# Kernel optimization log

Measured on AMD Instinct MI355X. Metric: run time of the kernel, lower is better.

Reference implementation:

```python
import jax, jax.numpy as jnp
import numpy as np

LEAK = 0.01  # torch F.leaky_relu default
EPS = 1e-5   # torch LayerNorm default


def _ln(x, g, b):
    mu = jnp.mean(x, axis=-1, keepdims=True)
    var = jnp.var(x, axis=-1, keepdims=True)
    return (x - mu) * jax.lax.rsqrt(var + EPS) * g + b


def setup_inputs() -> dict:
    key = jax.random.key(0)
    ks = jax.random.split(key, 12)
    npeds, h, e = 8192, 256, 64
    s = 0.05
    return {
        "last_pos": jax.random.normal(ks[0], (npeds, 2), jnp.float32),
        "last_pos_rel": jax.random.normal(ks[1], (npeds, 2), jnp.float32),
        "h0": jax.random.normal(ks[2], (1, npeds, h), jnp.float32) * s,
        "c0": jax.random.normal(ks[3], (1, npeds, h), jnp.float32) * s,
        "W_ih": jax.random.normal(ks[4], (4 * h, e), jnp.float32) * s,
        "W_hh": jax.random.normal(ks[5], (4 * h, h), jnp.float32) * s,
        "b_ih": jax.random.normal(ks[6], (4 * h,), jnp.float32) * s,
        "b_hh": jax.random.normal(ks[7], (4 * h,), jnp.float32) * s,
        "emb_W": jax.random.normal(ks[8], (e, 2), jnp.float32) * s,
        "emb_b": jax.random.normal(ks[9], (e,), jnp.float32) * s,
        "ln1_g": jnp.ones((2,), jnp.float32),
        "ln1_b": jnp.zeros((2,), jnp.float32),
        "pos_W": jax.random.normal(ks[10], (2, h), jnp.float32) * s,
        "pos_b": jax.random.normal(ks[11], (2,), jnp.float32) * s,
        "ln2_g": jnp.ones((h,), jnp.float32),
        "ln2_b": jnp.zeros((h,), jnp.float32),
    }


def reference(last_pos, last_pos_rel, h0, c0, W_ih, W_hh, b_ih, b_hh,
              emb_W, emb_b, ln1_g, ln1_b, pos_W, pos_b, ln2_g, ln2_b):
    seq_len = 30
    h_dim = W_hh.shape[1]
    bias = b_ih + b_hh

    def embed(p):  # leaky_relu(spatial_embedding(ln1(p)))
        return jax.nn.leaky_relu(_ln(p, ln1_g, ln1_b) @ emb_W.T + emb_b, LEAK)

    def step(carry, _):
        dec_in, h, c, lp = carry  # dec_in [N,e], h/c [N,H], lp [N,2]
        gates = dec_in @ W_ih.T + h @ W_hh.T + bias  # [N,4H]
        i, f, g, o = jnp.split(gates, 4, axis=-1)    # torch gate order i,f,g,o
        c = jax.nn.sigmoid(f) * c + jax.nn.sigmoid(i) * jnp.tanh(g)
        h = jax.nn.sigmoid(o) * jnp.tanh(c)
        rel = jax.nn.sigmoid(_ln(h, ln2_g, ln2_b) @ pos_W.T + pos_b)  # [N,2]
        lp = rel + lp
        return (embed(rel), h, c, lp), rel

    carry0 = (embed(last_pos_rel), h0[0], c0[0], last_pos)
    _, rels = jax.lax.scan(step, carry0, None, length=seq_len)
    return rels  # [seq_len, npeds, 2]
```

## Files before the change

kernel.cpp:

```cpp
#include <hip/hip_runtime.h>


typedef float  f32x4  __attribute__((ext_vector_type(4)));
typedef short  short8 __attribute__((ext_vector_type(8)));
typedef __bf16 bf16x8 __attribute__((ext_vector_type(8)));
typedef int    i32x4  __attribute__((ext_vector_type(4)));

#define WS_W     0
#define WS_HBUF  (640 * 1024)
#define WS_SBUF  (WS_HBUF + 8388608)
#define WS_BIAS  (WS_SBUF + 524288)
#define WS_SCAL  (WS_BIAS + 4096)
#define WS_CTR   (WS_SCAL + 64)

__device__ __forceinline__ unsigned short f2bf(float f) {
  unsigned int u = __float_as_uint(f);
  u += 0x7FFFu + ((u >> 16) & 1u);
  return (unsigned short)(u >> 16);
}
__device__ __forceinline__ float sigm(float x) {
  return __builtin_amdgcn_rcpf(1.0f + __expf(-x));
}
__device__ __forceinline__ float tanh_(float x) {
  float ax = fabsf(x);
  float t = __expf(-2.0f * ax);
  float r = (1.0f - t) * __builtin_amdgcn_rcpf(1.0f + t);
  return x >= 0.0f ? r : -r;
}
__device__ __forceinline__ f32x4 mfma16(short8 a, short8 b, f32x4 c) {
  return __builtin_amdgcn_mfma_f32_16x16x32_bf16(
      __builtin_bit_cast(bf16x8, a), __builtin_bit_cast(bf16x8, b), c, 0, 0, 0);
}
__device__ __forceinline__ void sc_store16(void* p, i32x4 v) {
  asm volatile("global_store_dwordx4 %0, %1, off sc0 sc1" ::"v"(p), "v"(v)
               : "memory");
}
__device__ __forceinline__ void drain_vm() {
  asm volatile("s_waitcnt vmcnt(0)" ::: "memory");
}
__device__ __forceinline__ void batch_load3(const i32x4* p0, const i32x4* p1,
                                            const i32x4* p2, i32x4& r0,
                                            i32x4& r1, i32x4& r2) {
  asm volatile(
      "global_load_dwordx4 %0, %3, off sc0 sc1\n\t"
      "global_load_dwordx4 %1, %4, off sc0 sc1\n\t"
      "global_load_dwordx4 %2, %5, off sc0 sc1\n\t"
      "s_waitcnt vmcnt(0)"
      : "=&v"(r0), "=&v"(r1), "=&v"(r2)
      : "v"(p0), "v"(p1), "v"(p2)
      : "memory");
}

extern "C" __global__ void shuffle_weights(const float* __restrict__ Wih,
                                           const float* __restrict__ Whh,
                                           unsigned short* __restrict__ ws_w) {
  int t = blockIdx.x * 256 + threadIdx.x;
  if (t >= 40960) return;
  int l = t & 63;
  int g = (t >> 6) & 3;
  int w8 = (t >> 8) & 7;
  int y = t >> 11;
  int kc = y % 10;
  int ug = y / 10;
  int row = g * 256 + ug * 128 + w8 * 16 + (l & 15);
  unsigned short* dst = ws_w + (size_t)t * 8;
  if (kc < 2) {
    const float* src = Wih + row * 64 + kc * 32 + (l >> 4) * 8;
#pragma unroll
    for (int j = 0; j < 8; j++) dst[j] = f2bf(src[j]);
  } else {
    const float* src = Whh + row * 256 + (kc - 2) * 32 + (l >> 4) * 8;
#pragma unroll
    for (int j = 0; j < 8; j++) dst[j] = f2bf(src[j]);
  }
}

extern "C" __global__ void prologue2(const float* __restrict__ b_ih,
                                     const float* __restrict__ b_hh,
                                     const float* __restrict__ ln2g,
                                     const float* __restrict__ ln2b,
                                     const float* __restrict__ posW,
                                     float* __restrict__ biasv,
                                     float* __restrict__ scal,
                                     int* __restrict__ ctr) {
  int t = threadIdx.x;
#pragma unroll
  for (int k2 = 0; k2 < 4; k2++) {
    int n = t * 4 + k2;
    biasv[n] = b_ih[n] + b_hh[n];
  }
  if (t < 128) ctr[t * 64] = 0;
  __shared__ float red[256][4];
  float g = ln2g[t], b = ln2b[t], p0 = posW[t], p1 = posW[256 + t];
  red[t][0] = b * p0;
  red[t][1] = b * p1;
  red[t][2] = g * p0;
  red[t][3] = g * p1;
  __syncthreads();
  for (int s = 128; s > 0; s >>= 1) {
    if (t < s) {
#pragma unroll
      for (int v = 0; v < 4; v++) red[t][v] += red[t + s][v];
    }
    __syncthreads();
  }
  if (t == 0) {
#pragma unroll
    for (int v = 0; v < 4; v++) scal[v] = red[0][v];
  }
}

extern "C" __global__ __launch_bounds__(512, 2) void decoder_main(
    const float* __restrict__ lpr, const float* __restrict__ h0,
    const float* __restrict__ c0, const float* __restrict__ embW,
    const float* __restrict__ embB, const float* __restrict__ ln1g,
    const float* __restrict__ ln1b, const float* __restrict__ posW,
    const float* __restrict__ posB, const float* __restrict__ ln2g,
    const unsigned short* __restrict__ ws_w,
    unsigned short* __restrict__ hbuf,
    float* __restrict__ sbuf,
    const float* __restrict__ biasv, const float* __restrict__ scal,
    int* __restrict__ ctr, float* __restrict__ out) {
  __shared__ unsigned short w_lds[3 * 8 * 4 * 512];
  __shared__ unsigned short h_stage[4 * 8 * 512];
  __shared__ unsigned short xh[4 * 2 * 512];
  __shared__ float partials[64 * 8 * 4];
  __shared__ float statl[64 * 4];
  __shared__ float n01[64][2];

  const int bid = blockIdx.x;
  const int pg = bid >> 1, ug = bid & 1;
  const int tid = threadIdx.x;
  const int w = tid >> 6, l = tid & 63;
  const int q = l >> 4, li = l & 15;
  const int P0 = pg * 64;
  const int loff = l * 8;
  const int u = ug * 128 + w * 16 + li;

  {
    const unsigned short* src = ws_w + (size_t)ug * 163840;
#pragma unroll
    for (int it = 0; it < 12; it++) {
      int f = tid + it * 512;
      *(short8*)(w_lds + f * 8) = *(const short8*)(src + f * 8);
    }
  }
  short8 wr[7][4];
#pragma unroll
  for (int kk = 0; kk < 7; kk++)
#pragma unroll
    for (int g = 0; g < 4; g++)
      wr[kk][g] = *(const short8*)(ws_w + (size_t)ug * 163840 +
                                   (((kk + 3) * 8 + w) * 4 + g) * 512 + loff);

  const float K0 = scal[0], K1 = scal[1], SP0 = scal[2], SP1 = scal[3];
  const float pb0 = posB[0], pb1 = posB[1];
  const float g10 = ln1g[0], g11 = ln1g[1], b10 = ln1b[0], b11 = ln1b[1];

  float bias_r[4];
#pragma unroll
  for (int g = 0; g < 4; g++) bias_r[g] = biasv[g * 256 + u];
  float Pp0, Pp1;
  {
    float gg = ln2g[u];
    Pp0 = gg * posW[u];
    Pp1 = gg * posW[256 + u];
  }

  f32x4 c_r[4];
#pragma unroll
  for (int mt = 0; mt < 4; mt++)
#pragma unroll
    for (int r = 0; r < 4; r++)
      c_r[mt][r] = c0[(size_t)(P0 + mt * 16 + q * 4 + r) * 256 + u];

#pragma unroll
  for (int it = 0; it < 4; it++) {
    int f = tid + it * 512;
    int ll = f & 63, kc = (f >> 6) & 7, Tl = f >> 9;
    const float* src =
        h0 + (size_t)(P0 + Tl * 16 + (ll & 15)) * 256 + kc * 32 + (ll >> 4) * 8;
    float tf[8];
    *(float4*)&tf[0] = *(const float4*)(src);
    *(float4*)&tf[4] = *(const float4*)(src + 4);
    short8 sv;
#pragma unroll
    for (int j = 0; j < 8; j++) sv[j] = (short)f2bf(tf[j]);
    *(short8*)(h_stage + f * 8) = sv;
  }

  if (tid < 64) {
    float r0 = lpr[(P0 + tid) * 2], r1 = lpr[(P0 + tid) * 2 + 1];
    float d = 0.5f * (r0 - r1);
    float rs = rsqrtf(d * d + 1e-5f);
    n01[tid][0] = d * rs * g10 + b10;
    n01[tid][1] = -d * rs * g11 + b11;
  }
  __syncthreads();

  {
    const int pc = tid >> 3, s8 = tid & 7;
    float n0 = n01[pc][0], n1 = n01[pc][1];
    int Tl = pc >> 4, row = pc & 15;
#pragma unroll
    for (int jj = 0; jj < 8; jj++) {
      int k = s8 * 8 + jj;
      float e = n0 * embW[k * 2] + n1 * embW[k * 2 + 1] + embB[k];
      e = e > 0.f ? e : 0.01f * e;
      xh[(Tl * 2 + (k >> 5)) * 512 + (row + 16 * ((k & 31) >> 3)) * 8 + (k & 7)] =
          f2bf(e);
    }
  }
  __syncthreads();

  i32x4* hb4 = (i32x4*)hbuf;
  i32x4* sb4 = (i32x4*)sbuf;
  i32x4* hs4 = (i32x4*)h_stage;
  const size_t own_base = ((size_t)pg * 2 + ug) * 1024;
  const size_t par_base = ((size_t)pg * 2 + (ug ^ 1)) * 1024;
  const size_t sown_base = ((size_t)pg * 2 + ug) * 64;
  const size_t spar_base = ((size_t)pg * 2 + (ug ^ 1)) * 64;

  for (int st = 0; st < 30; st++) {
    const size_t pbase = (size_t)(st & 1) * 262144;
    const size_t sbase = (size_t)(st & 1) * 16384;

    f32x4 acc[4][4];
#pragma unroll
    for (int g = 0; g < 4; g++)
#pragma unroll
      for (int mt = 0; mt < 4; mt++)
        acc[g][mt] = (f32x4){bias_r[g], bias_r[g], bias_r[g], bias_r[g]};

#pragma unroll
    for (int kc2 = 0; kc2 < 2; kc2++) {
      short8 ax[4];
#pragma unroll
      for (int mt = 0; mt < 4; mt++)
        ax[mt] = *(const short8*)(xh + (mt * 2 + kc2) * 512 + loff);
#pragma unroll
      for (int g = 0; g < 4; g++) {
        short8 b =
            *(const short8*)(w_lds + ((kc2 * 8 + w) * 4 + g) * 512 + loff);
#pragma unroll
        for (int mt = 0; mt < 4; mt++)
          acc[g][mt] = mfma16(ax[mt], b, acc[g][mt]);
      }
    }
#pragma unroll
    for (int kc = 0; kc < 8; kc++) {
      short8 a[4];
#pragma unroll
      for (int mt = 0; mt < 4; mt++)
        a[mt] = *(const short8*)(h_stage + (mt * 8 + kc) * 512 + loff);
      if (kc == 0) {
#pragma unroll
        for (int g = 0; g < 4; g++) {
          short8 b =
              *(const short8*)(w_lds + ((2 * 8 + w) * 4 + g) * 512 + loff);
#pragma unroll
          for (int mt = 0; mt < 4; mt++)
            acc[g][mt] = mfma16(a[mt], b, acc[g][mt]);
        }
      } else {
#pragma unroll
        for (int g = 0; g < 4; g++)
#pragma unroll
          for (int mt = 0; mt < 4; mt++)
            acc[g][mt] = mfma16(a[mt], wr[kc - 1][g], acc[g][mt]);
      }
    }
    __syncthreads();

#pragma unroll
    for (int mt = 0; mt < 4; mt++) {
      float sh[4], sh2[4], sA[4], sB[4];
#pragma unroll
      for (int r = 0; r < 4; r++) {
        float iv = sigm(acc[0][mt][r]);
        float fv = sigm(acc[1][mt][r]);
        float gv = tanh_(acc[2][mt][r]);
        float ov = sigm(acc[3][mt][r]);
        float cc = fv * c_r[mt][r] + iv * gv;
        c_r[mt][r] = cc;
        float hv = ov * tanh_(cc);
        h_stage[(mt * 8 + ug * 4 + (w >> 1)) * 512 +
                ((q * 4 + r) + 16 * ((w & 1) * 2 + (li >> 3))) * 8 + (li & 7)] =
            f2bf(hv);
        sh[r] = hv;
        sh2[r] = hv * hv;
        sA[r] = hv * Pp0;
        sB[r] = hv * Pp1;
      }
#pragma unroll
      for (int mask = 1; mask <= 8; mask <<= 1) {
#pragma unroll
        for (int r = 0; r < 4; r++) {
          sh[r] += __shfl_xor(sh[r], mask, 64);
          sh2[r] += __shfl_xor(sh2[r], mask, 64);
          sA[r] += __shfl_xor(sA[r], mask, 64);
          sB[r] += __shfl_xor(sB[r], mask, 64);
        }
      }
      if (li == 0) {
#pragma unroll
        for (int r = 0; r < 4; r++)
          *(f32x4*)(partials + ((mt * 16 + q * 4 + r) * 8 + w) * 4) =
              (f32x4){sh[r], sh2[r], sA[r], sB[r]};
      }
    }
    __syncthreads();

    f32x4 sown = (f32x4){0.f, 0.f, 0.f, 0.f};
    if (st < 29) {
#pragma unroll
      for (int it = 0; it < 2; it++) {
        int f = tid + it * 512;
        int c = f >> 6, rr = f & 63;
        int mt = c >> 2, kcl = c & 3;
        i32x4 v = hs4[(mt * 8 + ug * 4 + kcl) * 64 + rr];
        sc_store16(hb4 + pbase + own_base + f, v);
      }
    }
    if (tid < 64) {
      f32x4 sv = *(const f32x4*)(partials + tid * 32);
#pragma unroll
      for (int ww = 1; ww < 8; ww++) {
        f32x4 t2 = *(const f32x4*)(partials + (tid * 8 + ww) * 4);
        sv.x += t2.x; sv.y += t2.y; sv.z += t2.z; sv.w += t2.w;
      }
      sown = sv;
      sc_store16(sb4 + sbase + sown_base + tid, __builtin_bit_cast(i32x4, sv));
    }
    drain_vm();
    __syncthreads();

    if (tid == 0) {
      __hip_atomic_fetch_add(ctr + pg * 64, 1, __ATOMIC_RELAXED,
                             __HIP_MEMORY_SCOPE_AGENT);
      int target = 2 * (st + 1);
      while (__hip_atomic_load(ctr + pg * 64, __ATOMIC_RELAXED,
                               __HIP_MEMORY_SCOPE_AGENT) < target)
        __builtin_amdgcn_s_sleep(1);
    }
    __syncthreads();

    {
      const i32x4* p0 = hb4 + pbase + par_base + tid;
      const i32x4* p1 = p0 + 512;
      const i32x4* p2 =
          (tid < 64) ? (sb4 + sbase + spar_base + tid) : p0;
      i32x4 r0, r1, r2;
      batch_load3(p0, p1, p2, r0, r1, r2);
      if (st < 29) {
        int c0i = tid >> 6, rr = tid & 63;
        hs4[((c0i >> 2) * 8 + (ug ^ 1) * 4 + (c0i & 3)) * 64 + rr] = r0;
        int f1 = tid + 512;
        int c1 = f1 >> 6, rr1 = f1 & 63;
        hs4[((c1 >> 2) * 8 + (ug ^ 1) * 4 + (c1 & 3)) * 64 + rr1] = r1;
      }
      if (tid < 64) *(i32x4*)(statl + tid * 4) = __builtin_bit_cast(i32x4, r2);
    }
    __syncthreads();

    if (tid < 64) {
      f32x4 sp = *(const f32x4*)(statl + tid * 4);
      float S = sown.x + sp.x;
      float S2 = sown.y + sp.y;
      float D0 = sown.z + sp.z;
      float D1 = sown.w + sp.w;
      float mu = S * (1.0f / 256.0f);
      float var = S2 * (1.0f / 256.0f) - mu * mu;
      float rsig = rsqrtf(var + 1e-5f);
      float rel0 = sigm(rsig * (D0 - mu * SP0) + K0 + pb0);
      float rel1 = sigm(rsig * (D1 - mu * SP1) + K1 + pb1);
      if (ug == 0)
        *(float2*)(out + (size_t)st * 16384 + (P0 + tid) * 2) =
            make_float2(rel0, rel1);
      float d = 0.5f * (rel0 - rel1);
      float rs = rsqrtf(d * d + 1e-5f);
      n01[tid][0] = d * rs * g10 + b10;
      n01[tid][1] = -d * rs * g11 + b11;
    }
    __syncthreads();

    if (st < 29) {
      const int pc = tid >> 3, s8 = tid & 7;
      float n0 = n01[pc][0], n1 = n01[pc][1];
      int Tl = pc >> 4, row = pc & 15;
#pragma unroll
      for (int jj = 0; jj < 8; jj++) {
        int k = s8 * 8 + jj;
        float e = n0 * embW[k * 2] + n1 * embW[k * 2 + 1] + embB[k];
        e = e > 0.f ? e : 0.01f * e;
        xh[(Tl * 2 + (k >> 5)) * 512 + (row + 16 * ((k & 31) >> 3)) * 8 +
           (k & 7)] = f2bf(e);
      }
    }
    __syncthreads();
  }
}

extern "C" void kernel_launch(void* const* d_in, const int* in_sizes, int n_in,
                              void* d_out, int out_size, void* d_ws,
                              size_t ws_size, hipStream_t stream) {
  (void)in_sizes; (void)n_in; (void)out_size; (void)ws_size;
  const float* lpr  = (const float*)d_in[1];
  const float* h0   = (const float*)d_in[2];
  const float* c0   = (const float*)d_in[3];
  const float* Wih  = (const float*)d_in[4];
  const float* Whh  = (const float*)d_in[5];
  const float* b_ih = (const float*)d_in[6];
  const float* b_hh = (const float*)d_in[7];
  const float* embW = (const float*)d_in[8];
  const float* embB = (const float*)d_in[9];
  const float* ln1g = (const float*)d_in[10];
  const float* ln1b = (const float*)d_in[11];
  const float* posW = (const float*)d_in[12];
  const float* posB = (const float*)d_in[13];
  const float* ln2g = (const float*)d_in[14];
  const float* ln2b = (const float*)d_in[15];

  char* ws = (char*)d_ws;
  unsigned short* ws_w = (unsigned short*)(ws + WS_W);
  unsigned short* hbuf = (unsigned short*)(ws + WS_HBUF);
  float* sbufp  = (float*)(ws + WS_SBUF);
  float* biasv  = (float*)(ws + WS_BIAS);
  float* scal   = (float*)(ws + WS_SCAL);
  int*   ctr    = (int*)(ws + WS_CTR);

  shuffle_weights<<<dim3(160), dim3(256), 0, stream>>>(Wih, Whh, ws_w);
  prologue2<<<dim3(1), dim3(256), 0, stream>>>(b_ih, b_hh, ln2g, ln2b, posW,
                                               biasv, scal, ctr);
  decoder_main<<<dim3(256), dim3(512), 0, stream>>>(
      lpr, h0, c0, embW, embB, ln1g, ln1b, posW, posB, ln2g, ws_w, hbuf,
      sbufp, biasv, scal, ctr, (float*)d_out);
}
```

Before: 546.9 us.

## Give each block all hidden units for 32 peds, dropping cross-block exchange

```diff
diff --git a/kernel.cpp b/kernel.cpp
--- a/kernel.cpp
+++ b/kernel.cpp
@@ -4,14 +4,10 @@
 typedef float  f32x4  __attribute__((ext_vector_type(4)));
 typedef short  short8 __attribute__((ext_vector_type(8)));
 typedef __bf16 bf16x8 __attribute__((ext_vector_type(8)));
-typedef int    i32x4  __attribute__((ext_vector_type(4)));
 
 #define WS_W     0
-#define WS_HBUF  (640 * 1024)
-#define WS_SBUF  (WS_HBUF + 8388608)
-#define WS_BIAS  (WS_SBUF + 524288)
+#define WS_BIAS  (640 * 1024)
 #define WS_SCAL  (WS_BIAS + 4096)
-#define WS_CTR   (WS_SCAL + 64)
 
 __device__ __forceinline__ unsigned short f2bf(float f) {
   unsigned int u = __float_as_uint(f);
@@ -30,25 +26,6 @@
 __device__ __forceinline__ f32x4 mfma16(short8 a, short8 b, f32x4 c) {
   return __builtin_amdgcn_mfma_f32_16x16x32_bf16(
       __builtin_bit_cast(bf16x8, a), __builtin_bit_cast(bf16x8, b), c, 0, 0, 0);
-}
-__device__ __forceinline__ void sc_store16(void* p, i32x4 v) {
-  asm volatile("global_store_dwordx4 %0, %1, off sc0 sc1" ::"v"(p), "v"(v)
-               : "memory");
-}
-__device__ __forceinline__ void drain_vm() {
-  asm volatile("s_waitcnt vmcnt(0)" ::: "memory");
-}
-__device__ __forceinline__ void batch_load3(const i32x4* p0, const i32x4* p1,
-                                            const i32x4* p2, i32x4& r0,
-                                            i32x4& r1, i32x4& r2) {
-  asm volatile(
-      "global_load_dwordx4 %0, %3, off sc0 sc1\n\t"
-      "global_load_dwordx4 %1, %4, off sc0 sc1\n\t"
-      "global_load_dwordx4 %2, %5, off sc0 sc1\n\t"
-      "s_waitcnt vmcnt(0)"
-      : "=&v"(r0), "=&v"(r1), "=&v"(r2)
-      : "v"(p0), "v"(p1), "v"(p2)
-      : "memory");
 }
 
 extern "C" __global__ void shuffle_weights(const float* __restrict__ Wih,
@@ -57,22 +34,15 @@
   int t = blockIdx.x * 256 + threadIdx.x;
   if (t >= 40960) return;
   int l = t & 63;
-  int g = (t >> 6) & 3;
-  int w8 = (t >> 8) & 7;
-  int y = t >> 11;
-  int kc = y % 10;
-  int ug = y / 10;
-  int row = g * 256 + ug * 128 + w8 * 16 + (l & 15);
+  int nt = (t >> 6) & 63;
+  int kc = t >> 12;
+  int row = nt * 16 + (l & 15);
+  int cb = (l >> 4) * 8;
   unsigned short* dst = ws_w + (size_t)t * 8;
-  if (kc < 2) {
-    const float* src = Wih + row * 64 + kc * 32 + (l >> 4) * 8;
-#pragma unroll
-    for (int j = 0; j < 8; j++) dst[j] = f2bf(src[j]);
-  } else {
-    const float* src = Whh + row * 256 + (kc - 2) * 32 + (l >> 4) * 8;
-#pragma unroll
-    for (int j = 0; j < 8; j++) dst[j] = f2bf(src[j]);
-  }
+  const float* src = (kc < 2) ? (Wih + row * 64 + kc * 32 + cb)
+                              : (Whh + row * 256 + (kc - 2) * 32 + cb);
+#pragma unroll
+  for (int j = 0; j < 8; j++) dst[j] = f2bf(src[j]);
 }
 
 extern "C" __global__ void prologue2(const float* __restrict__ b_ih,
@@ -81,15 +51,13 @@
                                      const float* __restrict__ ln2b,
                                      const float* __restrict__ posW,
                                      float* __restrict__ biasv,
-                                     float* __restrict__ scal,
-                                     int* __restrict__ ctr) {
+                                     float* __restrict__ scal) {
   int t = threadIdx.x;
 #pragma unroll
   for (int k2 = 0; k2 < 4; k2++) {
     int n = t * 4 + k2;
     biasv[n] = b_ih[n] + b_hh[n];
   }
-  if (t < 128) ctr[t * 64] = 0;
   __shared__ float red[256][4];
   float g = ln2g[t], b = ln2b[t], p0 = posW[t], p1 = posW[256 + t];
   red[t][0] = b * p0;
@@ -117,69 +85,57 @@
     const float* __restrict__ ln1b, const float* __restrict__ posW,
     const float* __restrict__ posB, const float* __restrict__ ln2g,
     const unsigned short* __restrict__ ws_w,
-    unsigned short* __restrict__ hbuf,
-    float* __restrict__ sbuf,
     const float* __restrict__ biasv, const float* __restrict__ scal,
-    int* __restrict__ ctr, float* __restrict__ out) {
-  __shared__ unsigned short w_lds[3 * 8 * 4 * 512];
-  __shared__ unsigned short h_stage[4 * 8 * 512];
-  __shared__ unsigned short xh[4 * 2 * 512];
-  __shared__ float partials[64 * 8 * 4];
-  __shared__ float statl[64 * 4];
-  __shared__ float n01[64][2];
+    float* __restrict__ out) {
+  __shared__ unsigned short h_stage[16 * 512];
+  __shared__ unsigned short xh[4 * 512];
+  __shared__ float partials[32 * 8 * 4];
+  __shared__ float n01[32][2];
 
   const int bid = blockIdx.x;
-  const int pg = bid >> 1, ug = bid & 1;
   const int tid = threadIdx.x;
   const int w = tid >> 6, l = tid & 63;
   const int q = l >> 4, li = l & 15;
-  const int P0 = pg * 64;
+  const int P0 = bid * 32;
   const int loff = l * 8;
-  const int u = ug * 128 + w * 16 + li;
-
-  {
-    const unsigned short* src = ws_w + (size_t)ug * 163840;
-#pragma unroll
-    for (int it = 0; it < 12; it++) {
-      int f = tid + it * 512;
-      *(short8*)(w_lds + f * 8) = *(const short8*)(src + f * 8);
-    }
-  }
-  short8 wr[7][4];
-#pragma unroll
-  for (int kk = 0; kk < 7; kk++)
-#pragma unroll
-    for (int g = 0; g < 4; g++)
-      wr[kk][g] = *(const short8*)(ws_w + (size_t)ug * 163840 +
-                                   (((kk + 3) * 8 + w) * 4 + g) * 512 + loff);
+  const int u0 = w * 32 + li;
+
+  const unsigned short* wsw = ws_w + w * 1024 + loff;
 
   const float K0 = scal[0], K1 = scal[1], SP0 = scal[2], SP1 = scal[3];
   const float pb0 = posB[0], pb1 = posB[1];
   const float g10 = ln1g[0], g11 = ln1g[1], b10 = ln1b[0], b11 = ln1b[1];
 
-  float bias_r[4];
-#pragma unroll
-  for (int g = 0; g < 4; g++) bias_r[g] = biasv[g * 256 + u];
-  float Pp0, Pp1;
-  {
-    float gg = ln2g[u];
-    Pp0 = gg * posW[u];
-    Pp1 = gg * posW[256 + u];
-  }
-
-  f32x4 c_r[4];
-#pragma unroll
-  for (int mt = 0; mt < 4; mt++)
-#pragma unroll
-    for (int r = 0; r < 4; r++)
-      c_r[mt][r] = c0[(size_t)(P0 + mt * 16 + q * 4 + r) * 256 + u];
-
-#pragma unroll
-  for (int it = 0; it < 4; it++) {
+  float bias_r[4][2];
+#pragma unroll
+  for (int g = 0; g < 4; g++)
+#pragma unroll
+    for (int j = 0; j < 2; j++) bias_r[g][j] = biasv[g * 256 + u0 + j * 16];
+  float Pp0[2], Pp1[2];
+#pragma unroll
+  for (int j = 0; j < 2; j++) {
+    float gg = ln2g[u0 + j * 16];
+    Pp0[j] = gg * posW[u0 + j * 16];
+    Pp1[j] = gg * posW[256 + u0 + j * 16];
+  }
+
+  f32x4 c_r[2][2];
+#pragma unroll
+  for (int mt = 0; mt < 2; mt++)
+#pragma unroll
+    for (int j = 0; j < 2; j++)
+#pragma unroll
+      for (int r = 0; r < 4; r++)
+        c_r[mt][j][r] =
+            c0[(size_t)(P0 + mt * 16 + q * 4 + r) * 256 + u0 + j * 16];
+
+#pragma unroll
+  for (int it = 0; it < 2; it++) {
     int f = tid + it * 512;
-    int ll = f & 63, kc = (f >> 6) & 7, Tl = f >> 9;
-    const float* src =
-        h0 + (size_t)(P0 + Tl * 16 + (ll & 15)) * 256 + kc * 32 + (ll >> 4) * 8;
+    int ll = f & 63, fr = f >> 6;
+    int mt = fr >> 3, kc = fr & 7;
+    const float* src = h0 + (size_t)(P0 + mt * 16 + (ll & 15)) * 256 +
+                       kc * 32 + (ll >> 4) * 8;
     float tf[8];
     *(float4*)&tf[0] = *(const float4*)(src);
     *(float4*)&tf[4] = *(const float4*)(src + 4);
@@ -189,7 +145,7 @@
     *(short8*)(h_stage + f * 8) = sv;
   }
 
-  if (tid < 64) {
+  if (tid < 32) {
     float r0 = lpr[(P0 + tid) * 2], r1 = lpr[(P0 + tid) * 2 + 1];
     float d = 0.5f * (r0 - r1);
     float rs = rsqrtf(d * d + 1e-5f);
@@ -199,98 +155,91 @@
   __syncthreads();
 
   {
-    const int pc = tid >> 3, s8 = tid & 7;
+    const int pc = tid >> 4, s16 = tid & 15;
     float n0 = n01[pc][0], n1 = n01[pc][1];
-    int Tl = pc >> 4, row = pc & 15;
-#pragma unroll
-    for (int jj = 0; jj < 8; jj++) {
-      int k = s8 * 8 + jj;
+    int mt = pc >> 4, row = pc & 15;
+#pragma unroll
+    for (int jj = 0; jj < 4; jj++) {
+      int k = s16 * 4 + jj;
       float e = n0 * embW[k * 2] + n1 * embW[k * 2 + 1] + embB[k];
       e = e > 0.f ? e : 0.01f * e;
-      xh[(Tl * 2 + (k >> 5)) * 512 + (row + 16 * ((k & 31) >> 3)) * 8 + (k & 7)] =
-          f2bf(e);
+      xh[(mt * 2 + (k >> 5)) * 512 + (row + 16 * ((k & 31) >> 3)) * 8 +
+         (k & 7)] = f2bf(e);
     }
   }
   __syncthreads();
 
-  i32x4* hb4 = (i32x4*)hbuf;
-  i32x4* sb4 = (i32x4*)sbuf;
-  i32x4* hs4 = (i32x4*)h_stage;
-  const size_t own_base = ((size_t)pg * 2 + ug) * 1024;
-  const size_t par_base = ((size_t)pg * 2 + (ug ^ 1)) * 1024;
-  const size_t sown_base = ((size_t)pg * 2 + ug) * 64;
-  const size_t spar_base = ((size_t)pg * 2 + (ug ^ 1)) * 64;
+  short8 bb[2][4][2];
+#pragma unroll
+  for (int g = 0; g < 4; g++)
+#pragma unroll
+    for (int j = 0; j < 2; j++)
+      bb[0][g][j] = *(const short8*)(wsw + g * 8192 + j * 512);
 
   for (int st = 0; st < 30; st++) {
-    const size_t pbase = (size_t)(st & 1) * 262144;
-    const size_t sbase = (size_t)(st & 1) * 16384;
-
-    f32x4 acc[4][4];
-#pragma unroll
-    for (int g = 0; g < 4; g++)
-#pragma unroll
-      for (int mt = 0; mt < 4; mt++)
-        acc[g][mt] = (f32x4){bias_r[g], bias_r[g], bias_r[g], bias_r[g]};
-
-#pragma unroll
-    for (int kc2 = 0; kc2 < 2; kc2++) {
-      short8 ax[4];
-#pragma unroll
-      for (int mt = 0; mt < 4; mt++)
-        ax[mt] = *(const short8*)(xh + (mt * 2 + kc2) * 512 + loff);
-#pragma unroll
-      for (int g = 0; g < 4; g++) {
-        short8 b =
-            *(const short8*)(w_lds + ((kc2 * 8 + w) * 4 + g) * 512 + loff);
-#pragma unroll
-        for (int mt = 0; mt < 4; mt++)
-          acc[g][mt] = mfma16(ax[mt], b, acc[g][mt]);
-      }
-    }
-#pragma unroll
-    for (int kc = 0; kc < 8; kc++) {
-      short8 a[4];
-#pragma unroll
-      for (int mt = 0; mt < 4; mt++)
-        a[mt] = *(const short8*)(h_stage + (mt * 8 + kc) * 512 + loff);
-      if (kc == 0) {
-#pragma unroll
-        for (int g = 0; g < 4; g++) {
-          short8 b =
-              *(const short8*)(w_lds + ((2 * 8 + w) * 4 + g) * 512 + loff);
-#pragma unroll
-          for (int mt = 0; mt < 4; mt++)
-            acc[g][mt] = mfma16(a[mt], b, acc[g][mt]);
+    f32x4 acc[2][4][2];
+#pragma unroll
+    for (int mt = 0; mt < 2; mt++)
+#pragma unroll
+      for (int g = 0; g < 4; g++)
+#pragma unroll
+        for (int j = 0; j < 2; j++)
+          acc[mt][g][j] = (f32x4){bias_r[g][j], bias_r[g][j], bias_r[g][j],
+                                  bias_r[g][j]};
+
+#pragma unroll
+    for (int kc = 0; kc < 10; kc++) {
+      const int nkc = (kc == 9) ? 0 : kc + 1;
+      const unsigned short* wp = wsw + nkc * 32768;
+#pragma unroll
+      for (int g = 0; g < 4; g++)
+#pragma unroll
+        for (int j = 0; j < 2; j++)
+          bb[(kc + 1) & 1][g][j] = *(const short8*)(wp + g * 8192 + j * 512);
+      short8 a0, a1;
+      if (kc < 2) {
+        a0 = *(const short8*)(xh + kc * 512 + loff);
+        a1 = *(const short8*)(xh + (2 + kc) * 512 + loff);
+      } else {
+        a0 = *(const short8*)(h_stage + (kc - 2) * 512 + loff);
+        a1 = *(const short8*)(h_stage + (8 + kc - 2) * 512 + loff);
+      }
+#pragma unroll
+      for (int g = 0; g < 4; g++)
+#pragma unroll
+        for (int j = 0; j < 2; j++) {
+          acc[0][g][j] = mfma16(a0, bb[kc & 1][g][j], acc[0][g][j]);
+          acc[1][g][j] = mfma16(a1, bb[kc & 1][g][j], acc[1][g][j]);
         }
-      } else {
-#pragma unroll
-        for (int g = 0; g < 4; g++)
-#pragma unroll
-          for (int mt = 0; mt < 4; mt++)
-            acc[g][mt] = mfma16(a[mt], wr[kc - 1][g], acc[g][mt]);
-      }
-    }
-    __syncthreads();
-
-#pragma unroll
-    for (int mt = 0; mt < 4; mt++) {
+    }
+    __syncthreads();
+
+#pragma unroll
+    for (int mt = 0; mt < 2; mt++) {
       float sh[4], sh2[4], sA[4], sB[4];
 #pragma unroll
       for (int r = 0; r < 4; r++) {
-        float iv = sigm(acc[0][mt][r]);
-        float fv = sigm(acc[1][mt][r]);
-        float gv = tanh_(acc[2][mt][r]);
-        float ov = sigm(acc[3][mt][r]);
-        float cc = fv * c_r[mt][r] + iv * gv;
-        c_r[mt][r] = cc;
-        float hv = ov * tanh_(cc);
-        h_stage[(mt * 8 + ug * 4 + (w >> 1)) * 512 +
-                ((q * 4 + r) + 16 * ((w & 1) * 2 + (li >> 3))) * 8 + (li & 7)] =
-            f2bf(hv);
-        sh[r] = hv;
-        sh2[r] = hv * hv;
-        sA[r] = hv * Pp0;
-        sB[r] = hv * Pp1;
+        sh[r] = 0.f; sh2[r] = 0.f; sA[r] = 0.f; sB[r] = 0.f;
+      }
+#pragma unroll
+      for (int j = 0; j < 2; j++) {
+#pragma unroll
+        for (int r = 0; r < 4; r++) {
+          float iv = sigm(acc[mt][0][j][r]);
+          float fv = sigm(acc[mt][1][j][r]);
+          float gv = tanh_(acc[mt][2][j][r]);
+          float ov = sigm(acc[mt][3][j][r]);
+          float cc = fv * c_r[mt][j][r] + iv * gv;
+          c_r[mt][j][r] = cc;
+          float hv = ov * tanh_(cc);
+          h_stage[(mt * 8 + w) * 512 +
+                  ((q * 4 + r) + 16 * (j * 2 + (li >> 3))) * 8 + (li & 7)] =
+              f2bf(hv);
+          sh[r] += hv;
+          sh2[r] += hv * hv;
+          sA[r] += hv * Pp0[j];
+          sB[r] += hv * Pp1[j];
+        }
       }
 #pragma unroll
       for (int mask = 1; mask <= 8; mask <<= 1) {
@@ -311,72 +260,20 @@
     }
     __syncthreads();
 
-    f32x4 sown = (f32x4){0.f, 0.f, 0.f, 0.f};
-    if (st < 29) {
-#pragma unroll
-      for (int it = 0; it < 2; it++) {
-        int f = tid + it * 512;
-        int c = f >> 6, rr = f & 63;
-        int mt = c >> 2, kcl = c & 3;
-        i32x4 v = hs4[(mt * 8 + ug * 4 + kcl) * 64 + rr];
-        sc_store16(hb4 + pbase + own_base + f, v);
-      }
-    }
-    if (tid < 64) {
+    if (tid < 32) {
       f32x4 sv = *(const f32x4*)(partials + tid * 32);
 #pragma unroll
       for (int ww = 1; ww < 8; ww++) {
         f32x4 t2 = *(const f32x4*)(partials + (tid * 8 + ww) * 4);
         sv.x += t2.x; sv.y += t2.y; sv.z += t2.z; sv.w += t2.w;
       }
-      sown = sv;
-      sc_store16(sb4 + sbase + sown_base + tid, __builtin_bit_cast(i32x4, sv));
-    }
-    drain_vm();
-    __syncthreads();
-
-    if (tid == 0) {
-      __hip_atomic_fetch_add(ctr + pg * 64, 1, __ATOMIC_RELAXED,
-                             __HIP_MEMORY_SCOPE_AGENT);
-      int target = 2 * (st + 1);
-      while (__hip_atomic_load(ctr + pg * 64, __ATOMIC_RELAXED,
-                               __HIP_MEMORY_SCOPE_AGENT) < target)
-        __builtin_amdgcn_s_sleep(1);
-    }
-    __syncthreads();
-
-    {
-      const i32x4* p0 = hb4 + pbase + par_base + tid;
-      const i32x4* p1 = p0 + 512;
-      const i32x4* p2 =
-          (tid < 64) ? (sb4 + sbase + spar_base + tid) : p0;
-      i32x4 r0, r1, r2;
-      batch_load3(p0, p1, p2, r0, r1, r2);
-      if (st < 29) {
-        int c0i = tid >> 6, rr = tid & 63;
-        hs4[((c0i >> 2) * 8 + (ug ^ 1) * 4 + (c0i & 3)) * 64 + rr] = r0;
-        int f1 = tid + 512;
-        int c1 = f1 >> 6, rr1 = f1 & 63;
-        hs4[((c1 >> 2) * 8 + (ug ^ 1) * 4 + (c1 & 3)) * 64 + rr1] = r1;
-      }
-      if (tid < 64) *(i32x4*)(statl + tid * 4) = __builtin_bit_cast(i32x4, r2);
-    }
-    __syncthreads();
-
-    if (tid < 64) {
-      f32x4 sp = *(const f32x4*)(statl + tid * 4);
-      float S = sown.x + sp.x;
-      float S2 = sown.y + sp.y;
-      float D0 = sown.z + sp.z;
-      float D1 = sown.w + sp.w;
-      float mu = S * (1.0f / 256.0f);
-      float var = S2 * (1.0f / 256.0f) - mu * mu;
+      float mu = sv.x * (1.0f / 256.0f);
+      float var = sv.y * (1.0f / 256.0f) - mu * mu;
       float rsig = rsqrtf(var + 1e-5f);
-      float rel0 = sigm(rsig * (D0 - mu * SP0) + K0 + pb0);
-      float rel1 = sigm(rsig * (D1 - mu * SP1) + K1 + pb1);
-      if (ug == 0)
-        *(float2*)(out + (size_t)st * 16384 + (P0 + tid) * 2) =
-            make_float2(rel0, rel1);
+      float rel0 = sigm(rsig * (sv.z - mu * SP0) + K0 + pb0);
+      float rel1 = sigm(rsig * (sv.w - mu * SP1) + K1 + pb1);
+      *(float2*)(out + (size_t)st * 16384 + (P0 + tid) * 2) =
+          make_float2(rel0, rel1);
       float d = 0.5f * (rel0 - rel1);
       float rs = rsqrtf(d * d + 1e-5f);
       n01[tid][0] = d * rs * g10 + b10;
@@ -384,16 +281,16 @@
     }
     __syncthreads();
 
-    if (st < 29) {
-      const int pc = tid >> 3, s8 = tid & 7;
+    {
+      const int pc = tid >> 4, s16 = tid & 15;
       float n0 = n01[pc][0], n1 = n01[pc][1];
-      int Tl = pc >> 4, row = pc & 15;
-#pragma unroll
-      for (int jj = 0; jj < 8; jj++) {
-        int k = s8 * 8 + jj;
+      int mt = pc >> 4, row = pc & 15;
+#pragma unroll
+      for (int jj = 0; jj < 4; jj++) {
+        int k = s16 * 4 + jj;
         float e = n0 * embW[k * 2] + n1 * embW[k * 2 + 1] + embB[k];
         e = e > 0.f ? e : 0.01f * e;
-        xh[(Tl * 2 + (k >> 5)) * 512 + (row + 16 * ((k & 31) >> 3)) * 8 +
+        xh[(mt * 2 + (k >> 5)) * 512 + (row + 16 * ((k & 31) >> 3)) * 8 +
            (k & 7)] = f2bf(e);
       }
     }
@@ -423,16 +320,13 @@
 
   char* ws = (char*)d_ws;
   unsigned short* ws_w = (unsigned short*)(ws + WS_W);
-  unsigned short* hbuf = (unsigned short*)(ws + WS_HBUF);
-  float* sbufp  = (float*)(ws + WS_SBUF);
   float* biasv  = (float*)(ws + WS_BIAS);
   float* scal   = (float*)(ws + WS_SCAL);
-  int*   ctr    = (int*)(ws + WS_CTR);
 
   shuffle_weights<<<dim3(160), dim3(256), 0, stream>>>(Wih, Whh, ws_w);
   prologue2<<<dim3(1), dim3(256), 0, stream>>>(b_ih, b_hh, ln2g, ln2b, posW,
-                                               biasv, scal, ctr);
+                                               biasv, scal);
   decoder_main<<<dim3(256), dim3(512), 0, stream>>>(
-      lpr, h0, c0, embW, embB, ln1g, ln1b, posW, posB, ln2g, ws_w, hbuf,
-      sbufp, biasv, scal, ctr, (float*)d_out);
-}
+      lpr, h0, c0, embW, embB, ln1g, ln1b, posW, posB, ln2g, ws_w, biasv,
+      scal, (float*)d_out);
+}
```

Result: slower. 907.8 us (+66.0%).

## Overlap own-half recurrent MFMAs with partner exchange wait via per-block tags

Applied to the files above, without the earlier changes.

```diff
diff --git a/kernel.cpp b/kernel.cpp
--- a/kernel.cpp
+++ b/kernel.cpp
@@ -34,6 +34,12 @@
 __device__ __forceinline__ void sc_store16(void* p, i32x4 v) {
   asm volatile("global_store_dwordx4 %0, %1, off sc0 sc1" ::"v"(p), "v"(v)
                : "memory");
+}
+__device__ __forceinline__ void sc_load16(const i32x4* p, i32x4& r) {
+  asm volatile(
+      "global_load_dwordx4 %0, %1, off sc0 sc1\n\t"
+      "s_waitcnt vmcnt(0)"
+      : "=v"(r) : "v"(p) : "memory");
 }
 __device__ __forceinline__ void drain_vm() {
   asm volatile("s_waitcnt vmcnt(0)" ::: "memory");
@@ -89,7 +95,7 @@
     int n = t * 4 + k2;
     biasv[n] = b_ih[n] + b_hh[n];
   }
-  if (t < 128) ctr[t * 64] = 0;
+  ctr[t * 32] = 0;
   __shared__ float red[256][4];
   float g = ln2g[t], b = ln2b[t], p0 = posW[t], p1 = posW[256 + t];
   red[t][0] = b * p0;
@@ -109,6 +115,21 @@
     for (int v = 0; v < 4; v++) scal[v] = red[0][v];
   }
 }
+
+#define MF_STAGE(A0, A1, A2, A3, BGET)                                     \
+  {                                                                        \
+    short8 a0_ = (A0), a1_ = (A1), a2_ = (A2), a3_ = (A3);                 \
+    _Pragma("unroll") for (int g_ = 0; g_ < 4; g_++) {                     \
+      short8 b_ = (BGET);                                                  \
+      acc[g_][0] = mfma16(a0_, b_, acc[g_][0]);                            \
+      acc[g_][1] = mfma16(a1_, b_, acc[g_][1]);                            \
+      acc[g_][2] = mfma16(a2_, b_, acc[g_][2]);                            \
+      acc[g_][3] = mfma16(a3_, b_, acc[g_][3]);                            \
+    }                                                                      \
+  }
+#define HSA(kh, mt) (*(const short8*)(h_stage + ((mt)*8 + (kh)) * 512 + loff))
+#define XA(k2, mt)  (*(const short8*)(xh + ((mt)*2 + (k2)) * 512 + loff))
+#define WL(kc, g)   (*(const short8*)(w_lds + (((kc)*8 + w) * 4 + (g)) * 512 + loff))
 
 extern "C" __global__ __launch_bounds__(512, 2) void decoder_main(
     const float* __restrict__ lpr, const float* __restrict__ h0,
@@ -125,11 +146,11 @@
   __shared__ unsigned short h_stage[4 * 8 * 512];
   __shared__ unsigned short xh[4 * 2 * 512];
   __shared__ float partials[64 * 8 * 4];
-  __shared__ float statl[64 * 4];
   __shared__ float n01[64][2];
 
   const int bid = blockIdx.x;
-  const int pg = bid >> 1, ug = bid & 1;
+  const int ug = (bid >> 3) & 1;
+  const int pg = (bid & 7) | ((bid >> 4) << 3);
   const int tid = threadIdx.x;
   const int w = tid >> 6, l = tid & 63;
   const int q = l >> 4, li = l & 15;
@@ -180,12 +201,13 @@
     int ll = f & 63, kc = (f >> 6) & 7, Tl = f >> 9;
     const float* src =
         h0 + (size_t)(P0 + Tl * 16 + (ll & 15)) * 256 + kc * 32 + (ll >> 4) * 8;
-    float tf[8];
-    *(float4*)&tf[0] = *(const float4*)(src);
-    *(float4*)&tf[4] = *(const float4*)(src + 4);
+    float4 ta = *(const float4*)(src);
+    float4 tb = *(const float4*)(src + 4);
     short8 sv;
-#pragma unroll
-    for (int j = 0; j < 8; j++) sv[j] = (short)f2bf(tf[j]);
+    sv[0] = (short)f2bf(ta.x); sv[1] = (short)f2bf(ta.y);
+    sv[2] = (short)f2bf(ta.z); sv[3] = (short)f2bf(ta.w);
+    sv[4] = (short)f2bf(tb.x); sv[5] = (short)f2bf(tb.y);
+    sv[6] = (short)f2bf(tb.z); sv[7] = (short)f2bf(tb.w);
     *(short8*)(h_stage + f * 8) = sv;
   }
 
@@ -220,11 +242,11 @@
   const size_t par_base = ((size_t)pg * 2 + (ug ^ 1)) * 1024;
   const size_t sown_base = ((size_t)pg * 2 + ug) * 64;
   const size_t spar_base = ((size_t)pg * 2 + (ug ^ 1)) * 64;
+  int* tag_own = ctr + (pg * 2 + ug) * 32;
+  int* tag_par = ctr + (pg * 2 + (ug ^ 1)) * 32;
+  f32x4 sown = (f32x4){0.f, 0.f, 0.f, 0.f};
 
   for (int st = 0; st < 30; st++) {
-    const size_t pbase = (size_t)(st & 1) * 262144;
-    const size_t sbase = (size_t)(st & 1) * 16384;
-
     f32x4 acc[4][4];
 #pragma unroll
     for (int g = 0; g < 4; g++)
@@ -232,45 +254,86 @@
       for (int mt = 0; mt < 4; mt++)
         acc[g][mt] = (f32x4){bias_r[g], bias_r[g], bias_r[g], bias_r[g]};
 
-#pragma unroll
-    for (int kc2 = 0; kc2 < 2; kc2++) {
-      short8 ax[4];
-#pragma unroll
-      for (int mt = 0; mt < 4; mt++)
-        ax[mt] = *(const short8*)(xh + (mt * 2 + kc2) * 512 + loff);
-#pragma unroll
-      for (int g = 0; g < 4; g++) {
-        short8 b =
-            *(const short8*)(w_lds + ((kc2 * 8 + w) * 4 + g) * 512 + loff);
-#pragma unroll
-        for (int mt = 0; mt < 4; mt++)
-          acc[g][mt] = mfma16(ax[mt], b, acc[g][mt]);
-      }
-    }
-#pragma unroll
-    for (int kc = 0; kc < 8; kc++) {
-      short8 a[4];
-#pragma unroll
-      for (int mt = 0; mt < 4; mt++)
-        a[mt] = *(const short8*)(h_stage + (mt * 8 + kc) * 512 + loff);
-      if (kc == 0) {
-#pragma unroll
-        for (int g = 0; g < 4; g++) {
-          short8 b =
-              *(const short8*)(w_lds + ((2 * 8 + w) * 4 + g) * 512 + loff);
-#pragma unroll
-          for (int mt = 0; mt < 4; mt++)
-            acc[g][mt] = mfma16(a[mt], b, acc[g][mt]);
+    if (ug == 0) {
+      MF_STAGE(HSA(0, 0), HSA(0, 1), HSA(0, 2), HSA(0, 3), WL(2, g_));
+      MF_STAGE(HSA(1, 0), HSA(1, 1), HSA(1, 2), HSA(1, 3), wr[0][g_]);
+      MF_STAGE(HSA(2, 0), HSA(2, 1), HSA(2, 2), HSA(2, 3), wr[1][g_]);
+      MF_STAGE(HSA(3, 0), HSA(3, 1), HSA(3, 2), HSA(3, 3), wr[2][g_]);
+    } else {
+      MF_STAGE(HSA(4, 0), HSA(4, 1), HSA(4, 2), HSA(4, 3), wr[3][g_]);
+      MF_STAGE(HSA(5, 0), HSA(5, 1), HSA(5, 2), HSA(5, 3), wr[4][g_]);
+      MF_STAGE(HSA(6, 0), HSA(6, 1), HSA(6, 2), HSA(6, 3), wr[5][g_]);
+      MF_STAGE(HSA(7, 0), HSA(7, 1), HSA(7, 2), HSA(7, 3), wr[6][g_]);
+    }
+
+    if (st > 0) {
+      while (__hip_atomic_load(tag_par, __ATOMIC_RELAXED,
+                               __HIP_MEMORY_SCOPE_AGENT) < st)
+        __builtin_amdgcn_s_sleep(1);
+      const size_t pbase = (size_t)((st - 1) & 1) * 262144;
+      const size_t sbase = (size_t)((st - 1) & 1) * 16384;
+      const i32x4* p0 = hb4 + pbase + par_base + tid;
+      const i32x4* p1 = p0 + 512;
+      const i32x4* p2 = (tid < 64) ? (sb4 + sbase + spar_base + tid) : p0;
+      i32x4 r0, r1, r2;
+      batch_load3(p0, p1, p2, r0, r1, r2);
+      {
+        int c0i = tid >> 6, rr = tid & 63;
+        hs4[((c0i >> 2) * 8 + (ug ^ 1) * 4 + (c0i & 3)) * 64 + rr] = r0;
+        int f1 = tid + 512;
+        int c1 = f1 >> 6, rr1 = f1 & 63;
+        hs4[((c1 >> 2) * 8 + (ug ^ 1) * 4 + (c1 & 3)) * 64 + rr1] = r1;
+      }
+      if (tid < 64) {
+        f32x4 sp = __builtin_bit_cast(f32x4, r2);
+        float S = sown.x + sp.x;
+        float S2 = sown.y + sp.y;
+        float D0 = sown.z + sp.z;
+        float D1 = sown.w + sp.w;
+        float mu = S * (1.0f / 256.0f);
+        float var = S2 * (1.0f / 256.0f) - mu * mu;
+        float rsig = rsqrtf(var + 1e-5f);
+        float rel0 = sigm(rsig * (D0 - mu * SP0) + K0 + pb0);
+        float rel1 = sigm(rsig * (D1 - mu * SP1) + K1 + pb1);
+        if (ug == 0)
+          *(float2*)(out + (size_t)(st - 1) * 16384 + (P0 + tid) * 2) =
+              make_float2(rel0, rel1);
+        float d = 0.5f * (rel0 - rel1);
+        float rs = rsqrtf(d * d + 1e-5f);
+        n01[tid][0] = d * rs * g10 + b10;
+        n01[tid][1] = -d * rs * g11 + b11;
+      }
+      __syncthreads();
+      {
+        const int pc = tid >> 3, s8 = tid & 7;
+        float n0 = n01[pc][0], n1 = n01[pc][1];
+        int Tl = pc >> 4, row = pc & 15;
+#pragma unroll
+        for (int jj = 0; jj < 8; jj++) {
+          int k = s8 * 8 + jj;
+          float e = n0 * embW[k * 2] + n1 * embW[k * 2 + 1] + embB[k];
+          e = e > 0.f ? e : 0.01f * e;
+          xh[(Tl * 2 + (k >> 5)) * 512 + (row + 16 * ((k & 31) >> 3)) * 8 +
+             (k & 7)] = f2bf(e);
         }
-      } else {
-#pragma unroll
-        for (int g = 0; g < 4; g++)
-#pragma unroll
-          for (int mt = 0; mt < 4; mt++)
-            acc[g][mt] = mfma16(a[mt], wr[kc - 1][g], acc[g][mt]);
-      }
-    }
-    __syncthreads();
+      }
+      __syncthreads();
+    }
+
+    MF_STAGE(XA(0, 0), XA(0, 1), XA(0, 2), XA(0, 3), WL(0, g_));
+    MF_STAGE(XA(1, 0), XA(1, 1), XA(1, 2), XA(1, 3), WL(1, g_));
+    if (ug == 0) {
+      MF_STAGE(HSA(4, 0), HSA(4, 1), HSA(4, 2), HSA(4, 3), wr[3][g_]);
+      MF_STAGE(HSA(5, 0), HSA(5, 1), HSA(5, 2), HSA(5, 3), wr[4][g_]);
+      MF_STAGE(HSA(6, 0), HSA(6, 1), HSA(6, 2), HSA(6, 3), wr[5][g_]);
+      MF_STAGE(HSA(7, 0), HSA(7, 1), HSA(7, 2), HSA(7, 3), wr[6][g_]);
+    } else {
+      MF_STAGE(HSA(0, 0), HSA(0, 1), HSA(0, 2), HSA(0, 3), WL(2, g_));
+      MF_STAGE(HSA(1, 0), HSA(1, 1), HSA(1, 2), HSA(1, 3), wr[0][g_]);
+      MF_STAGE(HSA(2, 0), HSA(2, 1), HSA(2, 2), HSA(2, 3), wr[1][g_]);
+      MF_STAGE(HSA(3, 0), HSA(3, 1), HSA(3, 2), HSA(3, 3), wr[2][g_]);
+    }
+    if (st == 0) __syncthreads();
 
 #pragma unroll
     for (int mt = 0; mt < 4; mt++) {
@@ -311,93 +374,57 @@
     }
     __syncthreads();
 
-    f32x4 sown = (f32x4){0.f, 0.f, 0.f, 0.f};
-    if (st < 29) {
-#pragma unroll
-      for (int it = 0; it < 2; it++) {
-        int f = tid + it * 512;
-        int c = f >> 6, rr = f & 63;
-        int mt = c >> 2, kcl = c & 3;
-        i32x4 v = hs4[(mt * 8 + ug * 4 + kcl) * 64 + rr];
-        sc_store16(hb4 + pbase + own_base + f, v);
-      }
-    }
-    if (tid < 64) {
-      f32x4 sv = *(const f32x4*)(partials + tid * 32);
-#pragma unroll
-      for (int ww = 1; ww < 8; ww++) {
-        f32x4 t2 = *(const f32x4*)(partials + (tid * 8 + ww) * 4);
-        sv.x += t2.x; sv.y += t2.y; sv.z += t2.z; sv.w += t2.w;
-      }
-      sown = sv;
-      sc_store16(sb4 + sbase + sown_base + tid, __builtin_bit_cast(i32x4, sv));
-    }
-    drain_vm();
-    __syncthreads();
-
-    if (tid == 0) {
-      __hip_atomic_fetch_add(ctr + pg * 64, 1, __ATOMIC_RELAXED,
-                             __HIP_MEMORY_SCOPE_AGENT);
-      int target = 2 * (st + 1);
-      while (__hip_atomic_load(ctr + pg * 64, __ATOMIC_RELAXED,
-                               __HIP_MEMORY_SCOPE_AGENT) < target)
-        __builtin_amdgcn_s_sleep(1);
-    }
-    __syncthreads();
-
     {
-      const i32x4* p0 = hb4 + pbase + par_base + tid;
-      const i32x4* p1 = p0 + 512;
-      const i32x4* p2 =
-          (tid < 64) ? (sb4 + sbase + spar_base + tid) : p0;
-      i32x4 r0, r1, r2;
-      batch_load3(p0, p1, p2, r0, r1, r2);
+      const size_t pbase_w = (size_t)(st & 1) * 262144;
+      const size_t sbase_w = (size_t)(st & 1) * 16384;
       if (st < 29) {
-        int c0i = tid >> 6, rr = tid & 63;
-        hs4[((c0i >> 2) * 8 + (ug ^ 1) * 4 + (c0i & 3)) * 64 + rr] = r0;
-        int f1 = tid + 512;
-        int c1 = f1 >> 6, rr1 = f1 & 63;
-        hs4[((c1 >> 2) * 8 + (ug ^ 1) * 4 + (c1 & 3)) * 64 + rr1] = r1;
-      }
-      if (tid < 64) *(i32x4*)(statl + tid * 4) = __builtin_bit_cast(i32x4, r2);
-    }
-    __syncthreads();
-
-    if (tid < 64) {
-      f32x4 sp = *(const f32x4*)(statl + tid * 4);
-      float S = sown.x + sp.x;
-      float S2 = sown.y + sp.y;
-      float D0 = sown.z + sp.z;
-      float D1 = sown.w + sp.w;
-      float mu = S * (1.0f / 256.0f);
-      float var = S2 * (1.0f / 256.0f) - mu * mu;
-      float rsig = rsqrtf(var + 1e-5f);
-      float rel0 = sigm(rsig * (D0 - mu * SP0) + K0 + pb0);
-      float rel1 = sigm(rsig * (D1 - mu * SP1) + K1 + pb1);
-      if (ug == 0)
-        *(float2*)(out + (size_t)st * 16384 + (P0 + tid) * 2) =
-            make_float2(rel0, rel1);
-      float d = 0.5f * (rel0 - rel1);
-      float rs = rsqrtf(d * d + 1e-5f);
-      n01[tid][0] = d * rs * g10 + b10;
-      n01[tid][1] = -d * rs * g11 + b11;
-    }
-    __syncthreads();
-
-    if (st < 29) {
-      const int pc = tid >> 3, s8 = tid & 7;
-      float n0 = n01[pc][0], n1 = n01[pc][1];
-      int Tl = pc >> 4, row = pc & 15;
-#pragma unroll
-      for (int jj = 0; jj < 8; jj++) {
-        int k = s8 * 8 + jj;
-        float e = n0 * embW[k * 2] + n1 * embW[k * 2 + 1] + embB[k];
-        e = e > 0.f ? e : 0.01f * e;
-        xh[(Tl * 2 + (k >> 5)) * 512 + (row + 16 * ((k & 31) >> 3)) * 8 +
-           (k & 7)] = f2bf(e);
-      }
-    }
-    __syncthreads();
+#pragma unroll
+        for (int it = 0; it < 2; it++) {
+          int f = tid + it * 512;
+          int c = f >> 6, rr = f & 63;
+          int mt = c >> 2, kcl = c & 3;
+          i32x4 v = hs4[(mt * 8 + ug * 4 + kcl) * 64 + rr];
+          sc_store16(hb4 + pbase_w + own_base + f, v);
+        }
+      }
+      if (tid < 64) {
+        f32x4 sv = *(const f32x4*)(partials + tid * 32);
+#pragma unroll
+        for (int ww = 1; ww < 8; ww++) {
+          f32x4 t2 = *(const f32x4*)(partials + (tid * 8 + ww) * 4);
+          sv.x += t2.x; sv.y += t2.y; sv.z += t2.z; sv.w += t2.w;
+        }
+        sown = sv;
+        sc_store16(sb4 + sbase_w + sown_base + tid,
+                   __builtin_bit_cast(i32x4, sv));
+      }
+      drain_vm();
+      __syncthreads();
+      if (tid == 0)
+        __hip_atomic_store(tag_own, st + 1, __ATOMIC_RELAXED,
+                           __HIP_MEMORY_SCOPE_AGENT);
+    }
+  }
+
+  while (__hip_atomic_load(tag_par, __ATOMIC_RELAXED,
+                           __HIP_MEMORY_SCOPE_AGENT) < 30)
+    __builtin_amdgcn_s_sleep(1);
+  if (tid < 64) {
+    i32x4 r2;
+    sc_load16(sb4 + 16384 + spar_base + tid, r2);
+    f32x4 sp = __builtin_bit_cast(f32x4, r2);
+    float S = sown.x + sp.x;
+    float S2 = sown.y + sp.y;
+    float D0 = sown.z + sp.z;
+    float D1 = sown.w + sp.w;
+    float mu = S * (1.0f / 256.0f);
+    float var = S2 * (1.0f / 256.0f) - mu * mu;
+    float rsig = rsqrtf(var + 1e-5f);
+    float rel0 = sigm(rsig * (D0 - mu * SP0) + K0 + pb0);
+    float rel1 = sigm(rsig * (D1 - mu * SP1) + K1 + pb1);
+    if (ug == 0)
+      *(float2*)(out + (size_t)29 * 16384 + (P0 + tid) * 2) =
+          make_float2(rel0, rel1);
   }
 }
 
```

New measurement: 720.3 us. 1.32x slower.
